# Optimization experiments

Measured on AMD Instinct MI355X. Metric: run time of the kernel, lower is better.

Reference implementation:

```python
import jax, jax.numpy as jnp
import numpy as np

N_NODES = 100000
N_EDGES = 1600000
N_FEAT = 128
HIDDEN = 16
EMBED = 128
N_GRAPHS = 64


def setup_inputs() -> dict:
    key = jax.random.key(0)
    ks = jax.random.split(key, 6)
    x = jax.random.normal(ks[0], (N_NODES, N_FEAT), dtype=jnp.float32)
    edge_index = jax.random.randint(ks[1], (2, N_EDGES), 0, N_NODES, dtype=jnp.int32)
    batch = jnp.sort(jax.random.randint(ks[2], (N_NODES,), 0, N_GRAPHS, dtype=jnp.int32))
    W1 = jax.random.normal(ks[3], (N_FEAT, HIDDEN), dtype=jnp.float32) * (1.0 / np.sqrt(N_FEAT))
    b1 = jnp.zeros((HIDDEN,), dtype=jnp.float32)
    W2 = jax.random.normal(ks[4], (HIDDEN, EMBED), dtype=jnp.float32) * (1.0 / np.sqrt(HIDDEN))
    b2 = jnp.zeros((EMBED,), dtype=jnp.float32)
    return {"x": x, "edge_index": edge_index, "batch": batch,
            "W1": W1, "b1": b1, "W2": W2, "b2": b2}


def _gcn_conv(x, W, b, src, dst, dinv):
    # x' = D^{-1/2} (A + I) D^{-1/2} (x W) + b ; (src, dst) already include self-loops
    h = x @ W                                   # [N, out]
    norm = dinv[src] * dinv[dst]                # [E']
    msg = h[src] * norm[:, None]                # gather + scale
    out = jax.ops.segment_sum(msg, dst, num_segments=x.shape[0])  # scatter-add
    return out + b


def reference(x, edge_index, batch, W1, b1, W2, b2):
    n = x.shape[0]
    loop = jnp.arange(n, dtype=edge_index.dtype)
    src = jnp.concatenate([edge_index[0], loop])  # add self-loops
    dst = jnp.concatenate([edge_index[1], loop])
    deg = jax.ops.segment_sum(jnp.ones_like(dst, dtype=x.dtype), dst, num_segments=n)
    dinv = jnp.where(deg > 0, jax.lax.rsqrt(deg), 0.0)

    h = _gcn_conv(x, W1, b1, src, dst, dinv)
    h = jax.nn.relu(h)
    # dropout(p=0.2) is identity in eval mode
    h = _gcn_conv(h, W2, b2, src, dst, dinv)

    # mean pooling over graphs in the batch
    sums = jax.ops.segment_sum(h, batch, num_segments=N_GRAPHS)          # [G, EMBED]
    cnt = jax.ops.segment_sum(jnp.ones((n,), dtype=h.dtype), batch, num_segments=N_GRAPHS)
    return sums / jnp.maximum(cnt, 1.0)[:, None]
```

## Files before the change

### kernel.cpp

```cpp
#include <hip/hip_runtime.h>

#define HIDDEN 16
#define N_FEAT 128
#define EMBED 128
#define N_GRAPHS 64
#define BSH 8
#define MAXB 512

typedef unsigned int uint;

__device__ inline uint pk2(float a, float b) {
    uint ua = __float_as_uint(a), ub = __float_as_uint(b);
    ua = (ua + 0x7FFFu + ((ua >> 16) & 1u)) >> 16;
    ub = (ub + 0x7FFFu + ((ub >> 16) & 1u)) & 0xFFFF0000u;
    return ua | ub;
}
__device__ inline float2 upk2(uint w) {
    return make_float2(__uint_as_float(w << 16), __uint_as_float(w & 0xFFFF0000u));
}

__global__ void __launch_bounds__(1024)
k_hist(const int* __restrict__ dst, int n_edges, int nbuck, int* __restrict__ ghist) {
    __shared__ int h[MAXB];
    for (int i = threadIdx.x; i < MAXB; i += 1024) h[i] = 0;
    __syncthreads();
    int base = blockIdx.x * 4096;
#pragma unroll
    for (int j = 0; j < 4; j++) {
        int e = base + j * 1024 + threadIdx.x;
        if (e < n_edges) atomicAdd(&h[dst[e] >> BSH], 1);
    }
    __syncthreads();
    for (int b = threadIdx.x; b < nbuck; b += 1024)
        if (h[b]) atomicAdd(&ghist[b], h[b]);
}

__global__ void k_scan(const int* __restrict__ ghist, int nbuck,
                       int* __restrict__ gbase, int* __restrict__ gfill) {
    __shared__ int s[MAXB];
    int t = threadIdx.x;
    s[t] = (t < nbuck) ? ghist[t] : 0;
    __syncthreads();
    for (int st = 1; st < MAXB; st <<= 1) {
        int v = (t >= st) ? s[t - st] : 0;
        __syncthreads();
        s[t] += v;
        __syncthreads();
    }
    if (t < nbuck) {
        int excl = s[t] - ghist[t];
        gbase[t] = excl;
        gfill[t] = excl;
    }
}

__global__ void __launch_bounds__(1024)
k_part(const int* __restrict__ src, const int* __restrict__ dst,
       int n_edges, int nbuck, int* __restrict__ gfill, uint* __restrict__ ebuf) {
    __shared__ int hcnt[MAXB];
    __shared__ int hexcl[MAXB];
    __shared__ int hrank[MAXB];
    __shared__ int hbase[MAXB];
    __shared__ uint stage[4096];
    int tid = threadIdx.x;
    for (int i = tid; i < MAXB; i += 1024) { hcnt[i] = 0; hrank[i] = 0; }
    __syncthreads();
    int base = blockIdx.x * 4096;
    int cnt = min(4096, n_edges - base);
    int s_[4], d_[4];
#pragma unroll
    for (int j = 0; j < 4; j++) {
        int k = j * 1024 + tid;
        if (k < cnt) {
            s_[j] = src[base + k]; d_[j] = dst[base + k];
            atomicAdd(&hcnt[d_[j] >> BSH], 1);
        }
    }
    __syncthreads();
    if (tid < MAXB) hexcl[tid] = hcnt[tid];
    __syncthreads();
    for (int st = 1; st < MAXB; st <<= 1) {
        int v = 0;
        if (tid < MAXB && tid >= st) v = hexcl[tid - st];
        __syncthreads();
        if (tid < MAXB) hexcl[tid] += v;
        __syncthreads();
    }
    if (tid < nbuck && hcnt[tid] > 0)
        hbase[tid] = atomicAdd(&gfill[tid], hcnt[tid]);
    __syncthreads();
#pragma unroll
    for (int j = 0; j < 4; j++) {
        int k = j * 1024 + tid;
        if (k < cnt) {
            int b = d_[j] >> BSH;
            int r = atomicAdd(&hrank[b], 1);
            stage[hexcl[b] - hcnt[b] + r] = ((uint)s_[j] << 8) | ((uint)d_[j] & 255u);
        }
    }
    __syncthreads();
    for (int t = tid; t < cnt; t += 1024) {
        uint e = stage[t];
        int lo = 0, hi = MAXB - 1;
        while (lo < hi) {
            int mid = (lo + hi) >> 1;
            if (t < hexcl[mid]) hi = mid; else lo = mid + 1;
        }
        int b = lo;
        ebuf[hbase[b] + (t - (hexcl[b] - hcnt[b]))] = e;
    }
}

__global__ void __launch_bounds__(1024)
k_csr(const uint* __restrict__ ebuf, const int* __restrict__ gbase,
      const int* __restrict__ ghist, int n,
      int* __restrict__ deg, int* __restrict__ rowp, int* __restrict__ col) {
    __shared__ int nh[256], nexcl[256], nrank[256];
    int b = blockIdx.x;
    int tid = threadIdx.x;
    int seg0 = gbase[b];
    int cnt = ghist[b];
    int nb0 = b << BSH;
    if (tid < 256) { nh[tid] = 0; nrank[tid] = 0; }
    __syncthreads();
    for (int t = tid; t < cnt; t += 1024)
        atomicAdd(&nh[ebuf[seg0 + t] & 255u], 1);
    __syncthreads();
    if (tid < 256) nexcl[tid] = nh[tid];
    __syncthreads();
    for (int st = 1; st < 256; st <<= 1) {
        int v = 0;
        if (tid < 256 && tid >= st) v = nexcl[tid - st];
        __syncthreads();
        if (tid < 256) nexcl[tid] += v;
        __syncthreads();
    }
    if (tid < 256) {
        int node = nb0 + tid;
        if (node < n) {
            deg[node]  = nh[tid];
            rowp[node] = seg0 + nexcl[tid] - nh[tid];
        }
    }
    __syncthreads();
    for (int t = tid; t < cnt; t += 1024) {
        uint e = ebuf[seg0 + t];
        int ln = (int)(e & 255u);
        int r = atomicAdd(&nrank[ln], 1);
        col[seg0 + (nexcl[ln] - nh[ln]) + r] = (int)(e >> 8);
    }
}

__global__ void k_gemm1(const float* __restrict__ x, const float* __restrict__ W1,
                        const int* __restrict__ deg, float* __restrict__ dinv,
                        uint* __restrict__ Hs2, int n) {
    __shared__ float Ws[N_FEAT * HIDDEN];
    int tid = threadIdx.x;
    {
        const float4* w4 = (const float4*)W1;
        float4* s4 = (float4*)Ws;
        s4[tid * 2]     = w4[tid * 2];
        s4[tid * 2 + 1] = w4[tid * 2 + 1];
    }
    __syncthreads();
    int i = blockIdx.x * blockDim.x + tid;
    if (i >= n) return;

    float acc[HIDDEN];
#pragma unroll
    for (int o = 0; o < HIDDEN; o++) acc[o] = 0.f;

    const float4* xr = (const float4*)(x + (size_t)i * N_FEAT);
#pragma unroll 8
    for (int k4 = 0; k4 < N_FEAT / 4; k4++) {
        float4 xv = xr[k4];
        const float* w0 = &Ws[(k4 * 4 + 0) * HIDDEN];
        const float* w1 = &Ws[(k4 * 4 + 1) * HIDDEN];
        const float* w2 = &Ws[(k4 * 4 + 2) * HIDDEN];
        const float* w3 = &Ws[(k4 * 4 + 3) * HIDDEN];
#pragma unroll
        for (int o = 0; o < HIDDEN; o++)
            acc[o] += xv.x * w0[o] + xv.y * w1[o] + xv.z * w2[o] + xv.w * w3[o];
    }
    float di = rsqrtf((float)deg[i] + 1.0f);
    dinv[i] = di;
    uint o8[8];
#pragma unroll
    for (int j = 0; j < 8; j++) o8[j] = pk2(acc[2 * j] * di, acc[2 * j + 1] * di);
    uint4* hp = (uint4*)(Hs2 + (size_t)i * 8);
    hp[0] = make_uint4(o8[0], o8[1], o8[2], o8[3]);
    hp[1] = make_uint4(o8[4], o8[5], o8[6], o8[7]);
}

template <int LAYER>
__global__ void k_pull(const uint* __restrict__ V2, const int* __restrict__ rowptr,
                       const int* __restrict__ deg, const int* __restrict__ col,
                       const float* __restrict__ dinv, const float* __restrict__ b1,
                       uint* __restrict__ Q2, float2* __restrict__ R2, int n) {
    int wid = (blockIdx.x * blockDim.x + threadIdx.x) >> 6;
    int lane = threadIdx.x & 63;
    if (wid >= n) return;
    int f  = lane & 7;
    int es = lane >> 3;
    int start = rowptr[wid];
    int dg = deg[wid];
    float ax = 0.f, ay = 0.f;
    for (int j = es; j < dg; j += 8) {
        int s = col[start + j];
        float2 v = upk2(V2[(size_t)s * 8 + f]);
        ax += v.x; ay += v.y;
    }
    ax += __shfl_xor(ax, 8, 64);  ay += __shfl_xor(ay, 8, 64);
    ax += __shfl_xor(ax, 16, 64); ay += __shfl_xor(ay, 16, 64);
    ax += __shfl_xor(ax, 32, 64); ay += __shfl_xor(ay, 32, 64);
    if (lane < 8) {
        float2 h = upk2(V2[(size_t)wid * 8 + f]);
        float tx = ax + h.x, ty = ay + h.y;
        float di = dinv[wid];
        if (LAYER == 1) {
            float qa = fmaxf(di * tx + b1[2 * f],     0.f) * di;
            float qb = fmaxf(di * ty + b1[2 * f + 1], 0.f) * di;
            Q2[(size_t)wid * 8 + f] = pk2(qa, qb);
        } else {
            R2[(size_t)wid * 8 + f] = make_float2(di * tx, di * ty);
        }
    }
}

__global__ void k_pool(const float* __restrict__ R, const int* __restrict__ batch,
                       float* __restrict__ S, float* __restrict__ cnt, int n) {
    __shared__ float ls[8 * HIDDEN];
    __shared__ float lc[8];
    int tid = threadIdx.x;
    if (tid < 8) lc[tid] = 0.f;
    if (tid < 8 * HIDDEN) ls[tid] = 0.f;
    __syncthreads();

    int i0 = blockIdx.x * 256;
    int g0 = batch[i0 < n ? i0 : (n - 1)];
    int i = i0 + tid;
    if (i < n) {
        int g = batch[i];
        const float* r = R + (size_t)i * HIDDEN;
        int off = g - g0;
        if (off >= 0 && off < 8) {
#pragma unroll
            for (int o = 0; o < HIDDEN; o++) atomicAdd(&ls[off * HIDDEN + o], r[o]);
            atomicAdd(&lc[off], 1.f);
        } else {
#pragma unroll
            for (int o = 0; o < HIDDEN; o++) atomicAdd(&S[(size_t)g * HIDDEN + o], r[o]);
            atomicAdd(&cnt[g], 1.f);
        }
    }
    __syncthreads();
    if (tid < 8 * HIDDEN) {
        int b = tid >> 4, o = tid & 15;
        int g = g0 + b;
        float v = ls[b * HIDDEN + o];
        if (v != 0.f && g < N_GRAPHS) atomicAdd(&S[(size_t)g * HIDDEN + o], v);
    }
    if (tid < 8) {
        int g = g0 + tid;
        float c = lc[tid];
        if (c != 0.f && g < N_GRAPHS) atomicAdd(&cnt[g], c);
    }
}

__global__ void k_out(const float* __restrict__ S, const float* __restrict__ cnt,
                      const float* __restrict__ W2, const float* __restrict__ b2,
                      float* __restrict__ out) {
    int g = blockIdx.x;
    int e = threadIdx.x;
    float c = cnt[g];
    float acc = 0.f;
#pragma unroll
    for (int k = 0; k < HIDDEN; k++) acc += S[g * HIDDEN + k] * W2[k * EMBED + e];
    out[g * EMBED + e] = (c > 0.f) ? (acc / c + b2[e]) : 0.f;
}

extern "C" void kernel_launch(void* const* d_in, const int* in_sizes, int n_in,
                              void* d_out, int out_size, void* d_ws, size_t ws_size,
                              hipStream_t stream) {
    const float* x     = (const float*)d_in[0];
    const int*   ei    = (const int*)  d_in[1];
    const int*   batch = (const int*)  d_in[2];
    const float* W1    = (const float*)d_in[3];
    const float* b1    = (const float*)d_in[4];
    const float* W2    = (const float*)d_in[5];
    const float* b2    = (const float*)d_in[6];
    float* out = (float*)d_out;

    const int n       = in_sizes[2];
    const int n_edges = in_sizes[1] / 2;
    const int* srcp = ei;
    const int* dstp = ei + n_edges;
    const int nbuck = (n + 255) >> BSH;

    uint*  Hs2   = (uint*)d_ws;
    uint*  Q2    = Hs2 + (size_t)n * 8;
    float* dinv  = (float*)(Q2 + (size_t)n * 8);
    int*   deg   = (int*)(dinv + n);
    int*   rowp  = deg + n;
    int*   col   = rowp + n;
    uint*  ebuf  = (uint*)(col + n_edges);
    int*   ghist = (int*)(ebuf + n_edges);
    int*   gbase = ghist + MAXB;
    int*   gfill = gbase + MAXB;
    float* S     = (float*)(gfill + MAXB);
    float* cnt   = S + N_GRAPHS * HIDDEN;
    float* R     = (float*)ebuf;

    hipMemsetAsync(ghist, 0, MAXB * sizeof(int), stream);
    hipMemsetAsync(S, 0, (N_GRAPHS * HIDDEN + N_GRAPHS) * sizeof(float), stream);

    const int pb4k = (n_edges + 4095) / 4096;
    k_hist <<<pb4k, 1024, 0, stream>>>(dstp, n_edges, nbuck, ghist);
    k_scan <<<1, MAXB, 0, stream>>>(ghist, nbuck, gbase, gfill);
    k_part <<<pb4k, 1024, 0, stream>>>(srcp, dstp, n_edges, nbuck, gfill, ebuf);
    k_csr  <<<nbuck, 1024, 0, stream>>>(ebuf, gbase, ghist, n, deg, rowp, col);

    const int nb = (n + 255) / 256;
    k_gemm1<<<nb, 256, 0, stream>>>(x, W1, deg, dinv, Hs2, n);

    const int pullb = (n * 64 + 255) / 256;
    k_pull<1><<<pullb, 256, 0, stream>>>(Hs2, rowp, deg, col, dinv, b1, Q2, (float2*)R, n);
    k_pull<2><<<pullb, 256, 0, stream>>>(Q2,  rowp, deg, col, dinv, b1, Hs2, (float2*)R, n);

    k_pool <<<nb, 256, 0, stream>>>(R, batch, S, cnt, n);
    k_out  <<<N_GRAPHS, EMBED, 0, stream>>>(S, cnt, W2, b2, out);
}
```

Measured before the change: 255.1 us.

## Fuse CSR build into one cooperative kernel with grid syncs; store layer-2 output as bf16

Merges the histogram, scan, partition and per-bucket CSR kernels into a single cooperative launch separated by grid-wide syncs. Each block now handles 8192 edges with 512 threads, and a per-slot bucket array replaces the binary search. The two memsets become one. The layer-2 pull output is also packed to bf16 to halve its writes and the pool reads. In exchange, all blocks must be co-resident for the cooperative launch, and the extra bf16 rounding loses some precision.

```diff
diff --git a/kernel.cpp b/kernel.cpp
--- a/kernel.cpp
+++ b/kernel.cpp
@@ -1,4 +1,7 @@
 #include <hip/hip_runtime.h>
+#include <hip/hip_cooperative_groups.h>
+
+namespace cg = cooperative_groups;
 
 #define HIDDEN 16
 #define N_FEAT 128
@@ -6,6 +9,7 @@
 #define N_GRAPHS 64
 #define BSH 8
 #define MAXB 512
+#define EPT 16
 
 typedef unsigned int uint;
 
@@ -19,135 +23,121 @@
     return make_float2(__uint_as_float(w << 16), __uint_as_float(w & 0xFFFF0000u));
 }
 
-__global__ void __launch_bounds__(1024)
-k_hist(const int* __restrict__ dst, int n_edges, int nbuck, int* __restrict__ ghist) {
-    __shared__ int h[MAXB];
-    for (int i = threadIdx.x; i < MAXB; i += 1024) h[i] = 0;
-    __syncthreads();
-    int base = blockIdx.x * 4096;
-#pragma unroll
-    for (int j = 0; j < 4; j++) {
-        int e = base + j * 1024 + threadIdx.x;
-        if (e < n_edges) atomicAdd(&h[dst[e] >> BSH], 1);
-    }
-    __syncthreads();
-    for (int b = threadIdx.x; b < nbuck; b += 1024)
-        if (h[b]) atomicAdd(&ghist[b], h[b]);
-}
-
-__global__ void k_scan(const int* __restrict__ ghist, int nbuck,
-                       int* __restrict__ gbase, int* __restrict__ gfill) {
-    __shared__ int s[MAXB];
-    int t = threadIdx.x;
-    s[t] = (t < nbuck) ? ghist[t] : 0;
-    __syncthreads();
-    for (int st = 1; st < MAXB; st <<= 1) {
-        int v = (t >= st) ? s[t - st] : 0;
-        __syncthreads();
-        s[t] += v;
-        __syncthreads();
-    }
-    if (t < nbuck) {
-        int excl = s[t] - ghist[t];
-        gbase[t] = excl;
-        gfill[t] = excl;
-    }
-}
-
-__global__ void __launch_bounds__(1024)
-k_part(const int* __restrict__ src, const int* __restrict__ dst,
-       int n_edges, int nbuck, int* __restrict__ gfill, uint* __restrict__ ebuf) {
-    __shared__ int hcnt[MAXB];
-    __shared__ int hexcl[MAXB];
-    __shared__ int hrank[MAXB];
-    __shared__ int hbase[MAXB];
-    __shared__ uint stage[4096];
-    int tid = threadIdx.x;
-    for (int i = tid; i < MAXB; i += 1024) { hcnt[i] = 0; hrank[i] = 0; }
-    __syncthreads();
-    int base = blockIdx.x * 4096;
-    int cnt = min(4096, n_edges - base);
-    int s_[4], d_[4];
-#pragma unroll
-    for (int j = 0; j < 4; j++) {
-        int k = j * 1024 + tid;
+__global__ void __launch_bounds__(512, 4)
+k_build(const int* __restrict__ src, const int* __restrict__ dst,
+        int n_edges, int nbuck, int n,
+        int* __restrict__ ghist, int* __restrict__ gbase, int* __restrict__ gfill,
+        uint* __restrict__ ebuf,
+        int* __restrict__ deg, int* __restrict__ rowp, int* __restrict__ col) {
+    __shared__ int sh0[MAXB];
+    __shared__ int sh1[MAXB];
+    __shared__ int sh2[MAXB];
+    __shared__ int sh3[MAXB];
+    __shared__ uint stage[EPT * 512];
+    __shared__ unsigned short sbuck[EPT * 512];
+    cg::grid_group grid = cg::this_grid();
+    const int tid = threadIdx.x;
+    const int base = blockIdx.x * (EPT * 512);
+    const int cnt = min(EPT * 512, n_edges - base);
+    int s_[EPT], d_[EPT];
+
+    for (int i = tid; i < MAXB; i += 512) sh0[i] = 0;
+    __syncthreads();
+#pragma unroll
+    for (int j = 0; j < EPT; j++) {
+        int k = j * 512 + tid;
         if (k < cnt) {
             s_[j] = src[base + k]; d_[j] = dst[base + k];
-            atomicAdd(&hcnt[d_[j] >> BSH], 1);
-        }
-    }
-    __syncthreads();
-    if (tid < MAXB) hexcl[tid] = hcnt[tid];
-    __syncthreads();
-    for (int st = 1; st < MAXB; st <<= 1) {
-        int v = 0;
-        if (tid < MAXB && tid >= st) v = hexcl[tid - st];
-        __syncthreads();
-        if (tid < MAXB) hexcl[tid] += v;
-        __syncthreads();
-    }
-    if (tid < nbuck && hcnt[tid] > 0)
-        hbase[tid] = atomicAdd(&gfill[tid], hcnt[tid]);
-    __syncthreads();
-#pragma unroll
-    for (int j = 0; j < 4; j++) {
-        int k = j * 1024 + tid;
+            atomicAdd(&sh0[d_[j] >> BSH], 1);
+        }
+    }
+    __syncthreads();
+    for (int b = tid; b < nbuck; b += 512)
+        if (sh0[b]) atomicAdd(&ghist[b], sh0[b]);
+    grid.sync();
+
+    if (blockIdx.x == 0) {
+        int t = tid;
+        sh1[t] = (t < nbuck) ? ghist[t] : 0;
+        __syncthreads();
+        for (int st = 1; st < MAXB; st <<= 1) {
+            int v = (t >= st) ? sh1[t - st] : 0;
+            __syncthreads();
+            sh1[t] += v;
+            __syncthreads();
+        }
+        if (t < nbuck) {
+            int excl = sh1[t] - ghist[t];
+            gbase[t] = excl;
+            gfill[t] = excl;
+        }
+    }
+    grid.sync();
+
+    {
+        int t = tid;
+        sh1[t] = sh0[t];
+        __syncthreads();
+        for (int st = 1; st < MAXB; st <<= 1) {
+            int v = (t >= st) ? sh1[t - st] : 0;
+            __syncthreads();
+            sh1[t] += v;
+            __syncthreads();
+        }
+        sh2[t] = 0;
+        __syncthreads();
+        if (t < nbuck && sh0[t] > 0) sh3[t] = atomicAdd(&gfill[t], sh0[t]);
+        __syncthreads();
+    }
+#pragma unroll
+    for (int j = 0; j < EPT; j++) {
+        int k = j * 512 + tid;
         if (k < cnt) {
             int b = d_[j] >> BSH;
-            int r = atomicAdd(&hrank[b], 1);
-            stage[hexcl[b] - hcnt[b] + r] = ((uint)s_[j] << 8) | ((uint)d_[j] & 255u);
-        }
-    }
-    __syncthreads();
-    for (int t = tid; t < cnt; t += 1024) {
-        uint e = stage[t];
-        int lo = 0, hi = MAXB - 1;
-        while (lo < hi) {
-            int mid = (lo + hi) >> 1;
-            if (t < hexcl[mid]) hi = mid; else lo = mid + 1;
-        }
-        int b = lo;
-        ebuf[hbase[b] + (t - (hexcl[b] - hcnt[b]))] = e;
-    }
-}
-
-__global__ void __launch_bounds__(1024)
-k_csr(const uint* __restrict__ ebuf, const int* __restrict__ gbase,
-      const int* __restrict__ ghist, int n,
-      int* __restrict__ deg, int* __restrict__ rowp, int* __restrict__ col) {
-    __shared__ int nh[256], nexcl[256], nrank[256];
-    int b = blockIdx.x;
-    int tid = threadIdx.x;
-    int seg0 = gbase[b];
-    int cnt = ghist[b];
-    int nb0 = b << BSH;
-    if (tid < 256) { nh[tid] = 0; nrank[tid] = 0; }
-    __syncthreads();
-    for (int t = tid; t < cnt; t += 1024)
-        atomicAdd(&nh[ebuf[seg0 + t] & 255u], 1);
-    __syncthreads();
-    if (tid < 256) nexcl[tid] = nh[tid];
-    __syncthreads();
-    for (int st = 1; st < 256; st <<= 1) {
-        int v = 0;
-        if (tid < 256 && tid >= st) v = nexcl[tid - st];
-        __syncthreads();
-        if (tid < 256) nexcl[tid] += v;
-        __syncthreads();
-    }
-    if (tid < 256) {
-        int node = nb0 + tid;
-        if (node < n) {
-            deg[node]  = nh[tid];
-            rowp[node] = seg0 + nexcl[tid] - nh[tid];
-        }
-    }
-    __syncthreads();
-    for (int t = tid; t < cnt; t += 1024) {
-        uint e = ebuf[seg0 + t];
-        int ln = (int)(e & 255u);
-        int r = atomicAdd(&nrank[ln], 1);
-        col[seg0 + (nexcl[ln] - nh[ln]) + r] = (int)(e >> 8);
+            int r = atomicAdd(&sh2[b], 1);
+            int pos = sh1[b] - sh0[b] + r;
+            stage[pos] = ((uint)s_[j] << 8) | ((uint)d_[j] & 255u);
+            sbuck[pos] = (unsigned short)b;
+        }
+    }
+    __syncthreads();
+    for (int t = tid; t < cnt; t += 512) {
+        int b = sbuck[t];
+        ebuf[sh3[b] + (t - (sh1[b] - sh0[b]))] = stage[t];
+    }
+    grid.sync();
+
+    if (blockIdx.x < nbuck) {
+        int b = blockIdx.x;
+        int seg0 = gbase[b], c2 = ghist[b], nb0 = b << BSH;
+        if (tid < 256) { sh0[tid] = 0; sh2[tid] = 0; }
+        __syncthreads();
+        for (int t = tid; t < c2; t += 512)
+            atomicAdd(&sh0[ebuf[seg0 + t] & 255u], 1);
+        __syncthreads();
+        if (tid < 256) sh1[tid] = sh0[tid];
+        __syncthreads();
+        for (int st = 1; st < 256; st <<= 1) {
+            int v = 0;
+            if (tid < 256 && tid >= st) v = sh1[tid - st];
+            __syncthreads();
+            if (tid < 256) sh1[tid] += v;
+            __syncthreads();
+        }
+        if (tid < 256) {
+            int node = nb0 + tid;
+            if (node < n) {
+                deg[node]  = sh0[tid];
+                rowp[node] = seg0 + sh1[tid] - sh0[tid];
+            }
+        }
+        __syncthreads();
+        for (int t = tid; t < c2; t += 512) {
+            uint e = ebuf[seg0 + t];
+            int ln = (int)(e & 255u);
+            int r = atomicAdd(&sh2[ln], 1);
+            col[seg0 + (sh1[ln] - sh0[ln]) + r] = (int)(e >> 8);
+        }
     }
 }
 
@@ -196,7 +186,7 @@
 __global__ void k_pull(const uint* __restrict__ V2, const int* __restrict__ rowptr,
                        const int* __restrict__ deg, const int* __restrict__ col,
                        const float* __restrict__ dinv, const float* __restrict__ b1,
-                       uint* __restrict__ Q2, float2* __restrict__ R2, int n) {
+                       uint* __restrict__ out2, int n) {
     int wid = (blockIdx.x * blockDim.x + threadIdx.x) >> 6;
     int lane = threadIdx.x & 63;
     if (wid >= n) return;
@@ -220,14 +210,14 @@
         if (LAYER == 1) {
             float qa = fmaxf(di * tx + b1[2 * f],     0.f) * di;
             float qb = fmaxf(di * ty + b1[2 * f + 1], 0.f) * di;
-            Q2[(size_t)wid * 8 + f] = pk2(qa, qb);
+            out2[(size_t)wid * 8 + f] = pk2(qa, qb);
         } else {
-            R2[(size_t)wid * 8 + f] = make_float2(di * tx, di * ty);
-        }
-    }
-}
-
-__global__ void k_pool(const float* __restrict__ R, const int* __restrict__ batch,
+            out2[(size_t)wid * 8 + f] = pk2(di * tx, di * ty);
+        }
+    }
+}
+
+__global__ void k_pool(const uint* __restrict__ R2, const int* __restrict__ batch,
                        float* __restrict__ S, float* __restrict__ cnt, int n) {
     __shared__ float ls[8 * HIDDEN];
     __shared__ float lc[8];
@@ -241,7 +231,12 @@
     int i = i0 + tid;
     if (i < n) {
         int g = batch[i];
-        const float* r = R + (size_t)i * HIDDEN;
+        float r[HIDDEN];
+#pragma unroll
+        for (int j = 0; j < 8; j++) {
+            float2 v = upk2(R2[(size_t)i * 8 + j]);
+            r[2 * j] = v.x; r[2 * j + 1] = v.y;
+        }
         int off = g - g0;
         if (off >= 0 && off < 8) {
 #pragma unroll
@@ -291,11 +286,11 @@
     const float* b2    = (const float*)d_in[6];
     float* out = (float*)d_out;
 
-    const int n       = in_sizes[2];
-    const int n_edges = in_sizes[1] / 2;
+    int n       = in_sizes[2];
+    int n_edges = in_sizes[1] / 2;
     const int* srcp = ei;
     const int* dstp = ei + n_edges;
-    const int nbuck = (n + 255) >> BSH;
+    int nbuck = (n + 255) >> BSH;
 
     uint*  Hs2   = (uint*)d_ws;
     uint*  Q2    = Hs2 + (size_t)n * 8;
@@ -305,28 +300,30 @@
     int*   col   = rowp + n;
     uint*  ebuf  = (uint*)(col + n_edges);
     int*   ghist = (int*)(ebuf + n_edges);
-    int*   gbase = ghist + MAXB;
+    float* S     = (float*)(ghist + MAXB);
+    float* cnt   = S + N_GRAPHS * HIDDEN;
+    int*   gbase = (int*)(cnt + N_GRAPHS);
     int*   gfill = gbase + MAXB;
-    float* S     = (float*)(gfill + MAXB);
-    float* cnt   = S + N_GRAPHS * HIDDEN;
-    float* R     = (float*)ebuf;
-
-    hipMemsetAsync(ghist, 0, MAXB * sizeof(int), stream);
-    hipMemsetAsync(S, 0, (N_GRAPHS * HIDDEN + N_GRAPHS) * sizeof(float), stream);
-
-    const int pb4k = (n_edges + 4095) / 4096;
-    k_hist <<<pb4k, 1024, 0, stream>>>(dstp, n_edges, nbuck, ghist);
-    k_scan <<<1, MAXB, 0, stream>>>(ghist, nbuck, gbase, gfill);
-    k_part <<<pb4k, 1024, 0, stream>>>(srcp, dstp, n_edges, nbuck, gfill, ebuf);
-    k_csr  <<<nbuck, 1024, 0, stream>>>(ebuf, gbase, ghist, n, deg, rowp, col);
+    uint*  R2    = ebuf;
+
+    hipMemsetAsync(ghist, 0, (MAXB + N_GRAPHS * HIDDEN + N_GRAPHS) * sizeof(int), stream);
+
+    {
+        int pb8k = (n_edges + EPT * 512 - 1) / (EPT * 512);
+        int grid_b = nbuck > pb8k ? nbuck : pb8k;
+        void* args[] = {(void*)&srcp, (void*)&dstp, (void*)&n_edges, (void*)&nbuck,
+                        (void*)&n, (void*)&ghist, (void*)&gbase, (void*)&gfill,
+                        (void*)&ebuf, (void*)&deg, (void*)&rowp, (void*)&col};
+        hipLaunchCooperativeKernel((void*)k_build, dim3(grid_b), dim3(512), args, 0, stream);
+    }
 
     const int nb = (n + 255) / 256;
     k_gemm1<<<nb, 256, 0, stream>>>(x, W1, deg, dinv, Hs2, n);
 
     const int pullb = (n * 64 + 255) / 256;
-    k_pull<1><<<pullb, 256, 0, stream>>>(Hs2, rowp, deg, col, dinv, b1, Q2, (float2*)R, n);
-    k_pull<2><<<pullb, 256, 0, stream>>>(Q2,  rowp, deg, col, dinv, b1, Hs2, (float2*)R, n);
-
-    k_pool <<<nb, 256, 0, stream>>>(R, batch, S, cnt, n);
+    k_pull<1><<<pullb, 256, 0, stream>>>(Hs2, rowp, deg, col, dinv, b1, Q2, n);
+    k_pull<2><<<pullb, 256, 0, stream>>>(Q2,  rowp, deg, col, dinv, b1, R2, n);
+
+    k_pool <<<nb, 256, 0, stream>>>(R2, batch, S, cnt, n);
     k_out  <<<N_GRAPHS, EMBED, 0, stream>>>(S, cnt, W2, b2, out);
 }
```

Result: slower. 374.2 us (+46.7%).
